# Performance work log

Measured on AMD Instinct MI355X. Metric: run time of the kernel, lower is better.

The kernel has to match this reference:

```python
import jax, jax.numpy as jnp
import numpy as np


def setup_inputs() -> dict:
    key = jax.random.key(0)
    k1, k2 = jax.random.split(key)
    hidden = jax.random.normal(k1, (1, 64, 1024), dtype=jnp.float32)
    encoder_outputs = jax.random.normal(k2, (2048, 64, 1024), dtype=jnp.float32)
    return {"hidden": hidden, "encoder_outputs": encoder_outputs}


def reference(hidden, encoder_outputs):
    # hidden: [1, B, D]; encoder_outputs: [S, B, D]
    # energies[b, i] = dot(hidden[:, b], encoder_outputs[i, b])  (method='dot')
    energies = jnp.einsum('bd,sbd->bs', hidden[0], encoder_outputs)  # [B, S]
    attn = jax.nn.softmax(energies, axis=-1)  # F.softmax on 2D -> last dim
    return attn[:, None, :]  # [B, 1, S]
```

## Files before the change

kernel.cpp:

```cpp
#include <hip/hip_runtime.h>

#define SEQ 2048
#define BATCH 64
#define DIM 1024

__global__ __launch_bounds__(256) void energies_kernel(
    const float* __restrict__ hidden,
    const float* __restrict__ enc,
    float* __restrict__ out)
{
    const int wave = threadIdx.x >> 6;
    const int lane = threadIdx.x & 63;
    const int p = blockIdx.x * 4 + wave;
    const int b = p & (BATCH - 1);
    const int s = p >> 6;

    const float4* e4 = (const float4*)(enc + ((size_t)s * BATCH + b) * DIM);
    const float4* h4 = (const float4*)(hidden + (size_t)b * DIM);

    float acc = 0.f;
#pragma unroll
    for (int j = 0; j < 4; ++j) {
        float4 ev = e4[j * 64 + lane];
        float4 hv = h4[j * 64 + lane];
        acc += ev.x * hv.x + ev.y * hv.y + ev.z * hv.z + ev.w * hv.w;
    }

#pragma unroll
    for (int off = 32; off > 0; off >>= 1)
        acc += __shfl_down(acc, off, 64);

    if (lane == 0)
        out[(size_t)b * SEQ + s] = acc;
}

__global__ __launch_bounds__(256) void softmax_kernel(float* __restrict__ out)
{
    const int b = blockIdx.x;
    float* row = out + (size_t)b * SEQ;
    const int t = threadIdx.x;
    const int lane = t & 63;
    const int wv = t >> 6;

    __shared__ float red_max[4];
    __shared__ float red_sum[4];

    float v[8];
    float m = -INFINITY;
#pragma unroll
    for (int j = 0; j < 8; ++j) {
        v[j] = row[t + j * 256];
        m = fmaxf(m, v[j]);
    }
#pragma unroll
    for (int off = 1; off < 64; off <<= 1)
        m = fmaxf(m, __shfl_xor(m, off, 64));
    if (lane == 0) red_max[wv] = m;
    __syncthreads();
    m = fmaxf(fmaxf(red_max[0], red_max[1]), fmaxf(red_max[2], red_max[3]));

    float sum = 0.f;
#pragma unroll
    for (int j = 0; j < 8; ++j) {
        v[j] = __expf(v[j] - m);
        sum += v[j];
    }
#pragma unroll
    for (int off = 1; off < 64; off <<= 1)
        sum += __shfl_xor(sum, off, 64);
    if (lane == 0) red_sum[wv] = sum;
    __syncthreads();
    sum = (red_sum[0] + red_sum[1]) + (red_sum[2] + red_sum[3]);

    const float inv = 1.0f / sum;
#pragma unroll
    for (int j = 0; j < 8; ++j)
        row[t + j * 256] = v[j] * inv;
}

extern "C" void kernel_launch(void* const* d_in, const int* in_sizes, int n_in,
                              void* d_out, int out_size, void* d_ws, size_t ws_size,
                              hipStream_t stream) {
    const float* hidden = (const float*)d_in[0];
    const float* enc    = (const float*)d_in[1];
    float* out          = (float*)d_out;

    energies_kernel<<<(SEQ * BATCH) / 4, 256, 0, stream>>>(hidden, enc, out);
    softmax_kernel<<<BATCH, 256, 0, stream>>>(out);
}
```

Before: 664.1 us.

## Process multiple sequence rows per wave with hidden kept in registers

```diff
diff --git a/kernel.cpp b/kernel.cpp
--- a/kernel.cpp
+++ b/kernel.cpp
@@ -3,6 +3,14 @@
 #define SEQ 2048
 #define BATCH 64
 #define DIM 1024
+
+#define SPW 16
+#define WPB 4
+#define SPB (SPW * WPB)
+#define CHUNKS (SEQ / SPB)
+#define ROW_F4 (BATCH * DIM / 4)
+
+typedef float f4 __attribute__((ext_vector_type(4)));
 
 __global__ __launch_bounds__(256) void energies_kernel(
     const float* __restrict__ hidden,
@@ -11,27 +19,46 @@
 {
     const int wave = threadIdx.x >> 6;
     const int lane = threadIdx.x & 63;
-    const int p = blockIdx.x * 4 + wave;
-    const int b = p & (BATCH - 1);
-    const int s = p >> 6;
+    const int b     = blockIdx.x & (BATCH - 1);
+    const int chunk = blockIdx.x >> 6;
+    const int s_base = chunk * SPB + wave * SPW;
 
-    const float4* e4 = (const float4*)(enc + ((size_t)s * BATCH + b) * DIM);
-    const float4* h4 = (const float4*)(hidden + (size_t)b * DIM);
+    const f4* __restrict__ h4 = (const f4*)(hidden + (size_t)b * DIM);
+    const f4 h0 = h4[lane];
+    const f4 h1 = h4[64 + lane];
+    const f4 h2 = h4[128 + lane];
+    const f4 h3 = h4[192 + lane];
 
-    float acc = 0.f;
+    const f4* __restrict__ e0 =
+        (const f4*)(enc + ((size_t)s_base * BATCH + b) * DIM) + lane;
+
+    for (int i = 0; i < SPW; i += 4) {
+        float acc[4];
 #pragma unroll
-    for (int j = 0; j < 4; ++j) {
-        float4 ev = e4[j * 64 + lane];
-        float4 hv = h4[j * 64 + lane];
-        acc += ev.x * hv.x + ev.y * hv.y + ev.z * hv.z + ev.w * hv.w;
-    }
+        for (int u = 0; u < 4; ++u) {
+            const f4* __restrict__ e = e0 + (size_t)(i + u) * ROW_F4;
+            f4 a = __builtin_nontemporal_load(e);
+            f4 c = __builtin_nontemporal_load(e + 64);
+            f4 d = __builtin_nontemporal_load(e + 128);
+            f4 f = __builtin_nontemporal_load(e + 192);
+            acc[u] = a.x * h0.x + a.y * h0.y + a.z * h0.z + a.w * h0.w
+                   + c.x * h1.x + c.y * h1.y + c.z * h1.z + c.w * h1.w
+                   + d.x * h2.x + d.y * h2.y + d.z * h2.z + d.w * h2.w
+                   + f.x * h3.x + f.y * h3.y + f.z * h3.z + f.w * h3.w;
+        }
 
 #pragma unroll
-    for (int off = 32; off > 0; off >>= 1)
-        acc += __shfl_down(acc, off, 64);
+        for (int u = 0; u < 4; ++u) {
+#pragma unroll
+            for (int off = 32; off > 0; off >>= 1)
+                acc[u] += __shfl_xor(acc[u], off, 64);
+        }
 
-    if (lane == 0)
-        out[(size_t)b * SEQ + s] = acc;
+        if (lane == 0) {
+            f4 o = {acc[0], acc[1], acc[2], acc[3]};
+            *(f4*)(out + (size_t)b * SEQ + s_base + i) = o;
+        }
+    }
 }
 
 __global__ __launch_bounds__(256) void softmax_kernel(float* __restrict__ out)
@@ -85,6 +112,6 @@
     const float* enc    = (const float*)d_in[1];
     float* out          = (float*)d_out;
 
-    energies_kernel<<<(SEQ * BATCH) / 4, 256, 0, stream>>>(hidden, enc, out);
+    energies_kernel<<<CHUNKS * BATCH, 256, 0, stream>>>(hidden, enc, out);
     softmax_kernel<<<BATCH, 256, 0, stream>>>(out);
 }
```

After: 665.8 us. No clear change (+0.3%).
